# Optimization experiments

Measured on AMD Instinct MI355X. Metric: run time of the kernel, lower is better.

Reference implementation:

```python
import jax, jax.numpy as jnp
import numpy as np

EPS = 1e-5

def setup_inputs() -> dict:
    key = jax.random.key(0)
    k1, k2, k3, k4, k5 = jax.random.split(key, 5)
    N, E, D = 50000, 1600000, 128
    feat = jax.random.normal(k1, (N, D), dtype=jnp.float32)
    edge_index = jax.random.randint(k2, (2, E), 0, N, dtype=jnp.int64)
    W = jax.random.normal(k3, (D, D), dtype=jnp.float32) * (1.0 / np.sqrt(D))
    b = jax.random.normal(k4, (D,), dtype=jnp.float32) * 0.01
    gamma = jnp.ones((D,), dtype=jnp.float32)
    beta = jnp.zeros((D,), dtype=jnp.float32)
    return {"feat": feat, "edge_index": edge_index, "W": W, "b": b, "gamma": gamma, "beta": beta}

def reference(feat, edge_index, W, b, gamma, beta):
    # feat: [N, D] node features; edge_index: [2, E] (src, dst)
    N = feat.shape[0]
    src, dst = edge_index[0], edge_index[1]
    ones = jnp.ones(src.shape, dtype=feat.dtype)
    # out-degree of source nodes, in-degree of destination nodes
    deg_out = jnp.clip(jax.ops.segment_sum(ones, src, num_segments=N), 1.0)
    deg_in = jnp.clip(jax.ops.segment_sum(ones, dst, num_segments=N), 1.0)
    # pre-scale by D_out^{-1/2}, aggregate messages (copy_src + sum)
    feat_src = feat * jax.lax.rsqrt(deg_out)[:, None]        # [N, D]
    agg = jax.ops.segment_sum(feat_src[src], dst, num_segments=N)  # [N, D]
    # linear projection then post-scale by D_in^{-1/2}
    rst = agg @ W.T + b
    rst = rst * jax.lax.rsqrt(deg_in)[:, None]
    # identity residual (in_dim == out_dim)
    rst = rst + feat
    # LayerNorm(out_dim)
    mu = jnp.mean(rst, axis=-1, keepdims=True)
    var = jnp.var(rst, axis=-1, keepdims=True)
    rst = (rst - mu) * jax.lax.rsqrt(var + EPS) * gamma + beta
    # relu activation
    return jax.nn.relu(rst)
```

## Files before the change

### kernel.cpp

```cpp
#include <hip/hip_runtime.h>
#include <hip/hip_fp16.h>

#define LN_EPS 1e-5f
#define D 128
#define TN 16
#define BCAP 768
#define MAXB 4096
#define BBLK 128
#define HBLK 2048
#define NREP 8
#define AGG_LD 136

typedef _Float16 f16x4 __attribute__((ext_vector_type(4)));
typedef float f32x4 __attribute__((ext_vector_type(4)));

__global__ __launch_bounds__(256) void k_build(const int* __restrict__ ei, int E,
        int* __restrict__ cnt_out, int* __restrict__ bcnt,
        unsigned int* __restrict__ bkt, int NB, int Np) {
    __shared__ int h[MAXB];
    __shared__ int cur[MAXB];
    int tid = threadIdx.x;
    int E4 = E >> 2;
    const int4* src4 = (const int4*)ei;
    const int4* dst4 = (const int4*)(ei + E);

    if (blockIdx.x >= BBLK) {
        int* co = cnt_out + (size_t)(blockIdx.x & (NREP - 1)) * Np;
        int gtid = (blockIdx.x - BBLK) * 256 + tid;
        int gstride = (gridDim.x - BBLK) * 256;
        for (int i = gtid; i < E4; i += gstride) {
            int4 s = src4[i];
            atomicAdd(&co[s.x], 1);
            atomicAdd(&co[s.y], 1);
            atomicAdd(&co[s.z], 1);
            atomicAdd(&co[s.w], 1);
        }
        for (int e = (E4 << 2) + gtid; e < E; e += gstride) {
            atomicAdd(&co[ei[e]], 1);
        }
        return;
    }

    int chunk4 = (E4 + BBLK - 1) / BBLK;
    int lo4 = blockIdx.x * chunk4;
    int hi4 = min(E4, lo4 + chunk4);
    bool last = (blockIdx.x == BBLK - 1);

    for (int k = tid; k < NB; k += 256) h[k] = 0;
    __syncthreads();

    for (int i = lo4 + tid; i < hi4; i += 256) {
        int4 d = dst4[i];
        atomicAdd(&h[d.x >> 4], 1);
        atomicAdd(&h[d.y >> 4], 1);
        atomicAdd(&h[d.z >> 4], 1);
        atomicAdd(&h[d.w >> 4], 1);
    }
    if (last) {
        for (int e = (E4 << 2) + tid; e < E; e += 256)
            atomicAdd(&h[ei[E + e] >> 4], 1);
    }
    __syncthreads();

    for (int k = tid; k < NB; k += 256) {
        int c = h[k];
        cur[k] = c ? atomicAdd(&bcnt[k], c) : 0;
    }
    __syncthreads();

    for (int i = lo4 + tid; i < hi4; i += 256) {
        int4 s = src4[i];
        int4 d = dst4[i];
        int p0 = atomicAdd(&cur[d.x >> 4], 1);
        int p1 = atomicAdd(&cur[d.y >> 4], 1);
        int p2 = atomicAdd(&cur[d.z >> 4], 1);
        int p3 = atomicAdd(&cur[d.w >> 4], 1);
        if (p0 < BCAP) bkt[(size_t)(d.x >> 4) * BCAP + p0] = (unsigned)s.x | ((unsigned)(d.x & 15) << 16);
        if (p1 < BCAP) bkt[(size_t)(d.y >> 4) * BCAP + p1] = (unsigned)s.y | ((unsigned)(d.y & 15) << 16);
        if (p2 < BCAP) bkt[(size_t)(d.z >> 4) * BCAP + p2] = (unsigned)s.z | ((unsigned)(d.z & 15) << 16);
        if (p3 < BCAP) bkt[(size_t)(d.w >> 4) * BCAP + p3] = (unsigned)s.w | ((unsigned)(d.w & 15) << 16);
    }
    if (last) {
        for (int e = (E4 << 2) + tid; e < E; e += 256) {
            int s = ei[e], dd = ei[E + e];
            int p = atomicAdd(&cur[dd >> 4], 1);
            if (p < BCAP) bkt[(size_t)(dd >> 4) * BCAP + p] = (unsigned)s | ((unsigned)(dd & 15) << 16);
        }
    }
}

__global__ __launch_bounds__(256) void k_rs(const int* __restrict__ cnt_out,
                                            float* __restrict__ rs_out,
                                            const float* __restrict__ W,
                                            __half2* __restrict__ Wh2, int N, int Np) {
    int i = blockIdx.x * blockDim.x + threadIdx.x;
    if (i < N) {
        int so = 0;
        #pragma unroll
        for (int r = 0; r < NREP; ++r) so += cnt_out[(size_t)r * Np + i];
        rs_out[i] = rsqrtf((float)max(so, 1));
    }
    if (i < D * D / 2) {
        float2 w2 = ((const float2*)W)[i];
        Wh2[i] = __floats2half2_rn(w2.x, w2.y);
    }
}

__global__ __launch_bounds__(256) void k_prep(const float4* __restrict__ feat4,
                                              const float* __restrict__ rs_out,
                                              ushort4* __restrict__ feat_h,
                                              int total ) {
    int stride = gridDim.x * blockDim.x;
    for (int i = blockIdx.x * blockDim.x + threadIdx.x; i < total; i += stride) {
        int n = i >> 5;
        float rs = rs_out[n];
        float4 f = feat4[i];
        __half2 lo = __floats2half2_rn(f.x * rs, f.y * rs);
        __half2 hi = __floats2half2_rn(f.z * rs, f.w * rs);
        ushort4 u;
        u.x = __half_as_ushort(__low2half(lo));
        u.y = __half_as_ushort(__high2half(lo));
        u.z = __half_as_ushort(__low2half(hi));
        u.w = __half_as_ushort(__high2half(hi));
        feat_h[i] = u;
    }
}

__global__ __launch_bounds__(512) void k_fused(
        const int* __restrict__ bcnt, const unsigned int* __restrict__ bkt,
        const uint4* __restrict__ fh16, const _Float16* __restrict__ Wh,
        const float* __restrict__ bias, const float* __restrict__ gamma,
        const float* __restrict__ beta, const float* __restrict__ feat,
        float* __restrict__ out, int N) {
    __shared__ _Float16 aggH[TN * AGG_LD];
    __shared__ float redS[8][TN];
    __shared__ float redQ[8][TN];
    __shared__ unsigned int braw[BCAP];
    __shared__ unsigned short blist[BCAP];
    __shared__ int bstart[TN + 1];
    __shared__ int bfill[TN];
    __shared__ int bdeg[TN];

    int tid  = threadIdx.x;
    int wv   = tid >> 6;
    int lane = tid & 63;
    int l15  = lane & 15;
    int lg   = lane >> 4;

    int dA = wv * 16 + l15;
    float bd0 = bias[dA];
    float gd0 = gamma[dA];
    float bt0 = beta[dA];

    f16x4 Bf[8];
    #pragma unroll
    for (int kb = 0; kb < 8; ++kb)
        Bf[kb] = *reinterpret_cast<const f16x4*>(&Wh[(size_t)dA * D + kb * 16 + lg * 4]);

    int ntiles = (N + TN - 1) / TN;
    for (int t = blockIdx.x; t < ntiles; t += gridDim.x) {
        int nbase = t * TN;
        __syncthreads();

        if (tid < TN) { bdeg[tid] = 0; bfill[tid] = 0; }
        __syncthreads();
        int ecnt = min(bcnt[t], BCAP);
        for (int j = tid; j < ecnt; j += 512) {
            unsigned int v = bkt[(size_t)t * BCAP + j];
            braw[j] = v;
            atomicAdd(&bdeg[v >> 16], 1);
        }
        __syncthreads();
        if (tid == 0) {
            int run = 0;
            #pragma unroll
            for (int i = 0; i < TN; ++i) { bstart[i] = run; run += bdeg[i]; }
            bstart[TN] = run;
        }
        __syncthreads();
        for (int j = tid; j < ecnt; j += 512) {
            unsigned int v = braw[j];
            int node = v >> 16;
            int slot = bstart[node] + atomicAdd(&bfill[node], 1);
            blist[slot] = (unsigned short)(v & 0xFFFF);
        }
        __syncthreads();

        {
            int row  = wv * 2 + (lg & 1);
            int half = lg >> 1;
            int n    = nbase + row;
            float va[8];
            #pragma unroll
            for (int k = 0; k < 8; ++k) va[k] = 0.0f;
            if (n < N) {
                int deg = bdeg[row];
                int st  = bstart[row];
                int cnt = (deg > half) ? ((deg - half + 1) >> 1) : 0;
                int base = st + half;
                int j = 0;
                for (; j + 8 <= cnt; j += 8) {
                    int ss[8];
                    #pragma unroll
                    for (int k = 0; k < 8; ++k) ss[k] = blist[base + 2 * (j + k)];
                    uint4 vv[8];
                    #pragma unroll
                    for (int k = 0; k < 8; ++k) vv[k] = fh16[(size_t)ss[k] * 16 + l15];
                    #pragma unroll
                    for (int k = 0; k < 8; ++k) {
                        float2 f;
                        f = __half22float2(__builtin_bit_cast(__half2, vv[k].x));
                        va[0] += f.x; va[1] += f.y;
                        f = __half22float2(__builtin_bit_cast(__half2, vv[k].y));
                        va[2] += f.x; va[3] += f.y;
                        f = __half22float2(__builtin_bit_cast(__half2, vv[k].z));
                        va[4] += f.x; va[5] += f.y;
                        f = __half22float2(__builtin_bit_cast(__half2, vv[k].w));
                        va[6] += f.x; va[7] += f.y;
                    }
                }
                for (; j < cnt; ++j) {
                    int s = blist[base + 2 * j];
                    uint4 vv = fh16[(size_t)s * 16 + l15];
                    float2 f;
                    f = __half22float2(__builtin_bit_cast(__half2, vv.x)); va[0] += f.x; va[1] += f.y;
                    f = __half22float2(__builtin_bit_cast(__half2, vv.y)); va[2] += f.x; va[3] += f.y;
                    f = __half22float2(__builtin_bit_cast(__half2, vv.z)); va[4] += f.x; va[5] += f.y;
                    f = __half22float2(__builtin_bit_cast(__half2, vv.w)); va[6] += f.x; va[7] += f.y;
                }
            }
            #pragma unroll
            for (int k = 0; k < 8; ++k) va[k] += __shfl_xor(va[k], 32);
            if (half == 0) {
                __half2 h0 = __floats2half2_rn(va[0], va[1]);
                __half2 h1 = __floats2half2_rn(va[2], va[3]);
                __half2 h2 = __floats2half2_rn(va[4], va[5]);
                __half2 h3 = __floats2half2_rn(va[6], va[7]);
                uint4 o;
                o.x = __builtin_bit_cast(unsigned int, h0);
                o.y = __builtin_bit_cast(unsigned int, h1);
                o.z = __builtin_bit_cast(unsigned int, h2);
                o.w = __builtin_bit_cast(unsigned int, h3);
                *reinterpret_cast<uint4*>(&aggH[row * AGG_LD + l15 * 8]) = o;
            }
        }
        __syncthreads();

        f32x4 acc = {0.0f, 0.0f, 0.0f, 0.0f};
        #pragma unroll
        for (int kb = 0; kb < 8; ++kb) {
            f16x4 a = *reinterpret_cast<const f16x4*>(&aggH[l15 * AGG_LD + kb * 16 + lg * 4]);
            acc = __builtin_amdgcn_mfma_f32_16x16x16f16(a, Bf[kb], acc, 0, 0, 0);
        }

        float rv[4];
        #pragma unroll
        for (int r = 0; r < 4; ++r) {
            int m = lg * 4 + r;
            int n = nbase + m;
            float f0 = 0.0f;
            if (n < N) {
                float rsin = rsqrtf((float)max(bdeg[m], 1));
                f0 = (acc[r] + bd0) * rsin + feat[(size_t)n * D + dA];
            }
            rv[r] = f0;
            float s = f0;
            float q = f0 * f0;
            s += __shfl_xor(s, 1);  q += __shfl_xor(q, 1);
            s += __shfl_xor(s, 2);  q += __shfl_xor(q, 2);
            s += __shfl_xor(s, 4);  q += __shfl_xor(q, 4);
            s += __shfl_xor(s, 8);  q += __shfl_xor(q, 8);
            if (l15 == 0) { redS[wv][m] = s; redQ[wv][m] = q; }
        }
        __syncthreads();

        #pragma unroll
        for (int r = 0; r < 4; ++r) {
            int m = lg * 4 + r;
            int n = nbase + m;
            if (n < N) {
                float S = redS[0][m] + redS[1][m] + redS[2][m] + redS[3][m]
                        + redS[4][m] + redS[5][m] + redS[6][m] + redS[7][m];
                float Q = redQ[0][m] + redQ[1][m] + redQ[2][m] + redQ[3][m]
                        + redQ[4][m] + redQ[5][m] + redQ[6][m] + redQ[7][m];
                float mu  = S * (1.0f / 128.0f);
                float var = Q * (1.0f / 128.0f) - mu * mu;
                float inv = rsqrtf(var + LN_EPS);
                float v0 = (rv[r] - mu) * inv * gd0 + bt0;
                out[(size_t)n * D + dA] = fmaxf(v0, 0.0f);
            }
        }
    }
}

extern "C" void kernel_launch(void* const* d_in, const int* in_sizes, int n_in,
                              void* d_out, int out_size, void* d_ws, size_t ws_size,
                              hipStream_t stream) {
    const float* feat  = (const float*)d_in[0];
    const int*   ei    = (const int*)  d_in[1];
    const float* W     = (const float*)d_in[2];
    const float* bias  = (const float*)d_in[3];
    const float* gamma = (const float*)d_in[4];
    const float* beta  = (const float*)d_in[5];
    float* out = (float*)d_out;

    const int N  = in_sizes[0] / D;
    const int E  = in_sizes[1] / 2;
    const int NB = (N + TN - 1) / TN;

    const size_t Np  = ((size_t)N + 1023) & ~(size_t)1023;
    const size_t NBp = ((size_t)NB + 1023) & ~(size_t)1023;
    int*   cnt_out = (int*)d_ws;
    int*   bcnt    = cnt_out + NREP * Np;
    float* rs_out  = (float*)(bcnt + NBp);
    _Float16* Wh   = (_Float16*)(rs_out + Np);
    unsigned int* bkt = (unsigned int*)((int*)(rs_out + Np) + D * D / 2);
    ushort4* feat_h   = (ushort4*)(bkt + (size_t)NB * BCAP);

    hipMemsetAsync(d_ws, 0, (NREP * Np + NBp) * sizeof(int), stream);

    k_build<<<BBLK + HBLK, 256, 0, stream>>>(ei, E, cnt_out, bcnt, bkt, NB, (int)Np);
    int nblk = (max(N, D * D / 2) + 255) / 256;
    k_rs<<<nblk, 256, 0, stream>>>(cnt_out, rs_out, W, (__half2*)Wh, N, (int)Np);
    k_prep<<<2048, 256, 0, stream>>>((const float4*)feat, rs_out, feat_h, N * 32);
    k_fused<<<NB, 512, 0, stream>>>(bcnt, bkt,
                                    (const uint4*)feat_h, Wh, bias, gamma,
                                    beta, feat, out, N);
}
```

Measured before the change: 191.5 us.

## Persistent fused kernel with register-prefetched next-tile bucket loads

The fused aggregation kernel becomes persistent with a grid capped at 1024 blocks, instead of one block per tile. Each block loads the next tile's bucket entries and count into registers while it processes the current tile. The shared staging array is dropped, and the serial single-thread prefix sum is replaced with a 16-lane shuffle scan. The aim is to hide bucket load latency and cut per-tile setup serialization, at the cost of fewer resident blocks, since 3125 tiles now run on 1024 blocks in about three rounds.

```diff
diff --git a/kernel.cpp b/kernel.cpp
--- a/kernel.cpp
+++ b/kernel.cpp
@@ -10,6 +10,7 @@
 #define HBLK 2048
 #define NREP 8
 #define AGG_LD 136
+#define FGRID 1024
 
 typedef _Float16 f16x4 __attribute__((ext_vector_type(4)));
 typedef float f32x4 __attribute__((ext_vector_type(4)));
@@ -135,7 +136,6 @@
     __shared__ _Float16 aggH[TN * AGG_LD];
     __shared__ float redS[8][TN];
     __shared__ float redQ[8][TN];
-    __shared__ unsigned int braw[BCAP];
     __shared__ unsigned short blist[BCAP];
     __shared__ int bstart[TN + 1];
     __shared__ int bfill[TN];
@@ -158,31 +158,57 @@
         Bf[kb] = *reinterpret_cast<const f16x4*>(&Wh[(size_t)dA * D + kb * 16 + lg * 4]);
 
     int ntiles = (N + TN - 1) / TN;
-    for (int t = blockIdx.x; t < ntiles; t += gridDim.x) {
+
+    int t = blockIdx.x;
+    unsigned v0c = 0, v1c = 0;
+    int ec_c = 0;
+    if (t < ntiles) {
+        ec_c = min(bcnt[t], BCAP);
+        v0c = bkt[(size_t)t * BCAP + tid];
+        v1c = (tid + 512 < BCAP) ? bkt[(size_t)t * BCAP + tid + 512] : 0u;
+    }
+
+    for (; t < ntiles; t += gridDim.x) {
+        int t2 = t + gridDim.x;
+        unsigned v0n = 0, v1n = 0;
+        int ec_n = 0;
+        if (t2 < ntiles) {
+            ec_n = min(bcnt[t2], BCAP);
+            v0n = bkt[(size_t)t2 * BCAP + tid];
+            v1n = (tid + 512 < BCAP) ? bkt[(size_t)t2 * BCAP + tid + 512] : 0u;
+        }
+
         int nbase = t * TN;
         __syncthreads();
-
         if (tid < TN) { bdeg[tid] = 0; bfill[tid] = 0; }
         __syncthreads();
-        int ecnt = min(bcnt[t], BCAP);
-        for (int j = tid; j < ecnt; j += 512) {
-            unsigned int v = bkt[(size_t)t * BCAP + j];
-            braw[j] = v;
-            atomicAdd(&bdeg[v >> 16], 1);
-        }
-        __syncthreads();
-        if (tid == 0) {
-            int run = 0;
+
+        if (tid < ec_c)       atomicAdd(&bdeg[v0c >> 16], 1);
+        if (tid + 512 < ec_c) atomicAdd(&bdeg[v1c >> 16], 1);
+        __syncthreads();
+
+        if (tid < 16) {
+            int v = bdeg[tid];
+            int inc = v;
             #pragma unroll
-            for (int i = 0; i < TN; ++i) { bstart[i] = run; run += bdeg[i]; }
-            bstart[TN] = run;
-        }
-        __syncthreads();
-        for (int j = tid; j < ecnt; j += 512) {
-            unsigned int v = braw[j];
-            int node = v >> 16;
+            for (int off = 1; off < 16; off <<= 1) {
+                int u = __shfl_up(inc, off, 16);
+                if (tid >= off) inc += u;
+            }
+            bstart[tid] = inc - v;
+            if (tid == 15) bstart[16] = inc;
+        }
+        __syncthreads();
+
+        if (tid < ec_c) {
+            int node = v0c >> 16;
             int slot = bstart[node] + atomicAdd(&bfill[node], 1);
-            blist[slot] = (unsigned short)(v & 0xFFFF);
+            blist[slot] = (unsigned short)(v0c & 0xFFFF);
+        }
+        if (tid + 512 < ec_c) {
+            int node = v1c >> 16;
+            int slot = bstart[node] + atomicAdd(&bfill[node], 1);
+            blist[slot] = (unsigned short)(v1c & 0xFFFF);
         }
         __syncthreads();
 
@@ -290,6 +316,8 @@
                 out[(size_t)n * D + dA] = fmaxf(v0, 0.0f);
             }
         }
+
+        v0c = v0n; v1c = v1n; ec_c = ec_n;
     }
 }
 
@@ -323,7 +351,8 @@
     int nblk = (max(N, D * D / 2) + 255) / 256;
     k_rs<<<nblk, 256, 0, stream>>>(cnt_out, rs_out, W, (__half2*)Wh, N, (int)Np);
     k_prep<<<2048, 256, 0, stream>>>((const float4*)feat, rs_out, feat_h, N * 32);
-    k_fused<<<NB, 512, 0, stream>>>(bcnt, bkt,
-                                    (const uint4*)feat_h, Wh, bias, gamma,
-                                    beta, feat, out, N);
-}
+    int fgrid = (NB < FGRID) ? NB : FGRID;
+    k_fused<<<fgrid, 512, 0, stream>>>(bcnt, bkt,
+                                       (const uint4*)feat_h, Wh, bias, gamma,
+                                       beta, feat, out, N);
+}
```

New measurement: 181.5 us (median of 2 runs). -5.2%, faster.
